# Kernel tuning notes

Measured on AMD Instinct MI355X. Metric: run time of the kernel, lower is better.

The kernel has to match this reference:

```python
import jax, jax.numpy as jnp
import numpy as np

DECAY = 0.99
EPS = 1e-05
DIM = 64
N_EMBED = 512
X_SHAPE = (32, 4096, DIM)


def setup_inputs() -> dict:
    key = jax.random.key(0)
    k1, k2 = jax.random.split(key)
    x = jax.random.normal(k1, X_SHAPE, dtype=jnp.float32)
    # codebook init uniform(-1/n_embed, 1/n_embed), as in torch .uniform_
    embed = jax.random.uniform(k2, (DIM, N_EMBED), dtype=jnp.float32,
                               minval=-1.0 / N_EMBED, maxval=1.0 / N_EMBED)
    cluster_size = jnp.zeros((N_EMBED,), dtype=jnp.float32)
    embed_avg = embed.copy()
    return {"x": x, "embed": embed, "cluster_size": cluster_size, "embed_avg": embed_avg}


def reference(x, embed, cluster_size, embed_avg):
    dim, n_embed = embed.shape
    flatten = x.reshape(-1, dim)  # [N, dim]
    # squared euclidean distance to each code: ||f||^2 - 2 f.E + ||E||^2  -> [N, n_embed]
    dist = (jnp.sum(flatten * flatten, axis=1, keepdims=True)
            - 2.0 * (flatten @ embed)
            + jnp.sum(embed * embed, axis=0, keepdims=True))
    embed_ind_flat = jnp.argmin(dist, axis=1)  # [N]
    embed_ind = embed_ind_flat.reshape(x.shape[:-1])
    quantize = jnp.take(embed.T, embed_ind_flat, axis=0).reshape(x.shape)

    # --- training-mode EMA buffer updates (no gradient flows; torch uses .data) ---
    f_sg = jax.lax.stop_gradient(flatten)
    # onehot.sum(0) == histogram of assignments; flatten.T @ onehot == segment_sum
    onehot_sum = jnp.zeros((n_embed,), dtype=x.dtype).at[embed_ind_flat].add(1.0)
    embed_sum = jax.ops.segment_sum(f_sg, embed_ind_flat, num_segments=n_embed).T  # [dim, n_embed]
    new_cluster_size = cluster_size * DECAY + (1.0 - DECAY) * onehot_sum
    new_embed_avg = embed_avg * DECAY + (1.0 - DECAY) * embed_sum
    n = jnp.sum(new_cluster_size)
    cs = (new_cluster_size + EPS) / (n + n_embed * EPS) * n
    new_embed = new_embed_avg / cs[None, :]

    diff = jnp.mean(jnp.square(jax.lax.stop_gradient(quantize) - x))
    quantize_st = x + jax.lax.stop_gradient(quantize - x)  # straight-through
    return quantize_st, diff, embed_ind, new_embed, new_cluster_size, new_embed_avg
```

## Files before the change

### kernel.cpp

```cpp
#include <hip/hip_runtime.h>

#define NVEC  131072
#define DIM   64
#define K     512
#define DECAYF 0.99f
#define OMDF   0.01f
#define EPSF   1e-5f
#define VPB   128
#define NBLK_ASSIGN (NVEC / VPB)

#define Q_OFF    0
#define DIFF_OFF 8388608
#define IND_OFF  8388609
#define NE_OFF   8519681
#define NCS_OFF  8552449
#define NEA_OFF  8552961

#define ET_OFF    0
#define C_OFF     32768
#define DPART_OFF 33280
#define INDI_OFF  35328
#define PCNT_OFF  166400
#define PESUM_OFF 168448
#define NSH_OFF   299520

__global__ __launch_bounds__(256) void vq_prep(const float* __restrict__ embed,
                                               float* __restrict__ ws) {
    #pragma clang fp contract(off)
    int j = blockIdx.x * 256 + threadIdx.x;
    float c = 0.0f;
    for (int d = 0; d < DIM; ++d) {
        float v = embed[d * K + j];
        ws[ET_OFF + j * DIM + d] = v;
        float t = v * v;
        c = c + t;
    }
    ws[C_OFF + j] = c;
}

__global__ __launch_bounds__(256)
__attribute__((amdgpu_waves_per_eu(3)))
void vq_assign(
    const float* __restrict__ x,
    const float* __restrict__ ET,
    const float* __restrict__ C,
    int*   __restrict__ indI,
    float* __restrict__ dpart,
    float* __restrict__ out)
{
    #pragma clang fp contract(off)
    __shared__ float sda[4][64], sdb[4][64];
    __shared__ int   sia[4][64], sib[4][64];
    __shared__ int   sba[64], sbb[64];
    __shared__ float wdl[4];

    int lane = threadIdx.x & 63;
    int wq   = __builtin_amdgcn_readfirstlane(threadIdx.x >> 6);
    int va   = blockIdx.x * VPB + lane;
    int vb   = va + 64;
    const float* fxa = x + (size_t)va * DIM;
    const float* fxb = x + (size_t)vb * DIM;

    float fa[DIM], fb[DIM];
    #pragma unroll
    for (int k = 0; k < DIM / 4; ++k) {
        float4 t = ((const float4*)fxa)[k];
        fa[4*k+0] = t.x; fa[4*k+1] = t.y; fa[4*k+2] = t.z; fa[4*k+3] = t.w;
    }
    #pragma unroll
    for (int k = 0; k < DIM / 4; ++k) {
        float4 t = ((const float4*)fxb)[k];
        fb[4*k+0] = t.x; fb[4*k+1] = t.y; fb[4*k+2] = t.z; fb[4*k+3] = t.w;
    }

    #define PIN16(a, b) asm volatile("" \
        : "+v"(a[(b)+0]),  "+v"(a[(b)+1]),  "+v"(a[(b)+2]),  "+v"(a[(b)+3]), \
          "+v"(a[(b)+4]),  "+v"(a[(b)+5]),  "+v"(a[(b)+6]),  "+v"(a[(b)+7]), \
          "+v"(a[(b)+8]),  "+v"(a[(b)+9]),  "+v"(a[(b)+10]), "+v"(a[(b)+11]), \
          "+v"(a[(b)+12]), "+v"(a[(b)+13]), "+v"(a[(b)+14]), "+v"(a[(b)+15]))
    PIN16(fa, 0); PIN16(fa, 16); PIN16(fa, 32); PIN16(fa, 48);
    PIN16(fb, 0); PIN16(fb, 16); PIN16(fb, 32); PIN16(fb, 48);
    #undef PIN16

    float ra[8], rb[8];
    #pragma unroll
    for (int k = 0; k < 8; ++k) { ra[k] = fa[k] * fa[k]; rb[k] = fb[k] * fb[k]; }
    #pragma unroll
    for (int b = 1; b < 8; ++b) {
        #pragma unroll
        for (int k = 0; k < 8; ++k) {
            float t0 = fa[8*b + k] * fa[8*b + k];
            ra[k] = ra[k] + t0;
            float t1 = fb[8*b + k] * fb[8*b + k];
            rb[k] = rb[k] + t1;
        }
    }
    float Aa = ((ra[0] + ra[1]) + (ra[2] + ra[3])) + ((ra[4] + ra[5]) + (ra[6] + ra[7]));
    float Ab = ((rb[0] + rb[1]) + (rb[2] + rb[3])) + ((rb[4] + rb[5]) + (rb[6] + rb[7]));

    const float* eseg = ET + (size_t)wq * 128 * DIM;
    const float* Cseg = C + wq * 128;
    float bda = 3.0e38f, bdb = 3.0e38f;
    int   bia = wq * 128, bib = wq * 128;
    #pragma unroll 1
    for (int jj = 0; jj < 128; ++jj) {
        const float* e = eseg + jj * DIM;
        float ma = 0.0f, mb = 0.0f;
        #pragma unroll
        for (int d = 0; d < DIM; ++d) {
            float ev = e[d];
            ma = __builtin_fmaf(fa[d], ev, ma);
            mb = __builtin_fmaf(fb[d], ev, mb);
        }
        int j = wq * 128 + jj;
        float Cv = Cseg[jj];
        float t1a = 2.0f * ma;
        float t2a = Aa - t1a;
        float da  = t2a + Cv;
        float t1b = 2.0f * mb;
        float t2b = Ab - t1b;
        float db  = t2b + Cv;
        if (da < bda) { bda = da; bia = j; }
        if (db < bdb) { bdb = db; bib = j; }
    }

    sda[wq][lane] = bda; sia[wq][lane] = bia;
    sdb[wq][lane] = bdb; sib[wq][lane] = bib;
    __syncthreads();

    if (wq == 0) {
        float bd = sda[0][lane]; int bi = sia[0][lane];
        #pragma unroll
        for (int q = 1; q < 4; ++q) {
            float d2 = sda[q][lane]; int i2 = sia[q][lane];
            if (d2 < bd || (d2 == bd && i2 < bi)) { bd = d2; bi = i2; }
        }
        sba[lane] = bi;
        out[IND_OFF + va] = (float)bi;
        indI[va] = bi;

        bd = sdb[0][lane]; bi = sib[0][lane];
        #pragma unroll
        for (int q = 1; q < 4; ++q) {
            float d2 = sdb[q][lane]; int i2 = sib[q][lane];
            if (d2 < bd || (d2 == bd && i2 < bi)) { bd = d2; bi = i2; }
        }
        sbb[lane] = bi;
        out[IND_OFF + vb] = (float)bi;
        indI[vb] = bi;
    }
    __syncthreads();

    float dl = 0.0f;
    if (wq == 0) {
        int bsel = sba[lane];
        const float4* qr = (const float4*)(ET + (size_t)bsel * DIM);
        float4* orow = (float4*)(out + Q_OFF + (size_t)va * DIM);
        #pragma unroll
        for (int k = 0; k < 16; ++k) {
            float4 tq = qr[k];
            float r0 = tq.x - fa[4*k+0];
            float r1 = tq.y - fa[4*k+1];
            float r2 = tq.z - fa[4*k+2];
            float r3 = tq.w - fa[4*k+3];
            dl = __builtin_fmaf(r0, r0, dl); dl = __builtin_fmaf(r1, r1, dl);
            dl = __builtin_fmaf(r2, r2, dl); dl = __builtin_fmaf(r3, r3, dl);
            orow[k] = tq;
        }
    } else if (wq == 1) {
        int bsel = sbb[lane];
        const float4* qr = (const float4*)(ET + (size_t)bsel * DIM);
        float4* orow = (float4*)(out + Q_OFF + (size_t)vb * DIM);
        #pragma unroll
        for (int k = 0; k < 16; ++k) {
            float4 tq = qr[k];
            float r0 = tq.x - fb[4*k+0];
            float r1 = tq.y - fb[4*k+1];
            float r2 = tq.z - fb[4*k+2];
            float r3 = tq.w - fb[4*k+3];
            dl = __builtin_fmaf(r0, r0, dl); dl = __builtin_fmaf(r1, r1, dl);
            dl = __builtin_fmaf(r2, r2, dl); dl = __builtin_fmaf(r3, r3, dl);
            orow[k] = tq;
        }
    }

    #pragma unroll
    for (int off = 32; off > 0; off >>= 1) dl += __shfl_down(dl, off);
    if (lane == 0) wdl[wq] = dl;
    __syncthreads();
    if (threadIdx.x == 0)
        dpart[blockIdx.x] = ((wdl[0] + wdl[1]) + (wdl[2] + wdl[3]));
}

__global__ __launch_bounds__(512) void vq_stats(
    const float* __restrict__ x,
    const int* __restrict__ indI,
    float* __restrict__ pcnt,
    float* __restrict__ pesum)
{
    __shared__ float p[4][8][DIM];
    __shared__ float c[4][8];
    int jg   = blockIdx.x >> 2;
    int q    = blockIdx.x & 3;
    int lane = threadIdx.x & 63;
    int w    = __builtin_amdgcn_readfirstlane(threadIdx.x >> 6);
    int j0   = jg * 4;

    int seg  = q * 8 + w;
    int base = seg * (NVEC / 32);

    float acc[4] = {0.0f, 0.0f, 0.0f, 0.0f};
    int   cnt[4] = {0, 0, 0, 0};
    for (int i = 0; i < NVEC / 32; i += 256) {
        int4 idv = ((const int4*)(indI + base + i))[lane];
        #pragma unroll
        for (int jj = 0; jj < 4; ++jj) {
            int j = j0 + jj;
            unsigned long long m0 = __ballot(idv.x == j);
            unsigned long long m1 = __ballot(idv.y == j);
            unsigned long long m2 = __ballot(idv.z == j);
            unsigned long long m3 = __ballot(idv.w == j);
            cnt[jj] += (int)(__popcll(m0) + __popcll(m1)
                           + __popcll(m2) + __popcll(m3));
            while (m0) { int b = __builtin_ctzll(m0); m0 &= m0 - 1;
                         acc[jj] += x[(size_t)(base + i + 4*b + 0) * DIM + lane]; }
            while (m1) { int b = __builtin_ctzll(m1); m1 &= m1 - 1;
                         acc[jj] += x[(size_t)(base + i + 4*b + 1) * DIM + lane]; }
            while (m2) { int b = __builtin_ctzll(m2); m2 &= m2 - 1;
                         acc[jj] += x[(size_t)(base + i + 4*b + 2) * DIM + lane]; }
            while (m3) { int b = __builtin_ctzll(m3); m3 &= m3 - 1;
                         acc[jj] += x[(size_t)(base + i + 4*b + 3) * DIM + lane]; }
        }
    }
    #pragma unroll
    for (int jj = 0; jj < 4; ++jj) {
        p[jj][w][lane] = acc[jj];
        if (lane == 0) c[jj][w] = (float)cnt[jj];
    }
    __syncthreads();
    if (w == 0) {
        #pragma unroll
        for (int jj = 0; jj < 4; ++jj) {
            float s = ((p[jj][0][lane] + p[jj][1][lane])
                     + (p[jj][2][lane] + p[jj][3][lane]))
                    + ((p[jj][4][lane] + p[jj][5][lane])
                     + (p[jj][6][lane] + p[jj][7][lane]));
            pesum[((size_t)q * K + (j0 + jj)) * DIM + lane] = s;
            if (lane == 0)
                pcnt[q * K + (j0 + jj)] =
                    ((c[jj][0] + c[jj][1]) + (c[jj][2] + c[jj][3]))
                  + ((c[jj][4] + c[jj][5]) + (c[jj][6] + c[jj][7]));
        }
    }
}

__global__ __launch_bounds__(512) void vq_finalize(
    const float* __restrict__ cluster_size,
    const float* __restrict__ embed_avg,
    const float* __restrict__ ws,
    float* __restrict__ out)
{
    __shared__ float wsum[8];
    __shared__ float dsum_sh[8];
    __shared__ float n_sh;
    int d = blockIdx.x;
    int j = threadIdx.x;

    float cj = ((ws[PCNT_OFF + 0*K + j] + ws[PCNT_OFF + 1*K + j])
              + (ws[PCNT_OFF + 2*K + j] + ws[PCNT_OFF + 3*K + j]));
    float ncs = DECAYF * cluster_size[j] + OMDF * cj;
    if (d == 0) out[NCS_OFF + j] = ncs;

    float dsum = 0.0f;
    if (d == 0) {
        #pragma unroll
        for (int k = 0; k < NBLK_ASSIGN / 512; ++k)
            dsum += ws[DPART_OFF + k * 512 + j];
    }

    float s = ncs;
    #pragma unroll
    for (int off = 32; off > 0; off >>= 1) {
        s    += __shfl_down(s, off);
        dsum += __shfl_down(dsum, off);
    }
    if ((j & 63) == 0) { wsum[j >> 6] = s; dsum_sh[j >> 6] = dsum; }
    __syncthreads();
    if (j == 0) {
        float n = 0.f, dtot = 0.f;
        #pragma unroll
        for (int w = 0; w < 8; ++w) { n += wsum[w]; dtot += dsum_sh[w]; }
        n_sh = n;
        if (d == 0) out[DIFF_OFF] = dtot * (1.0f / 8388608.0f);
    }
    __syncthreads();
    float n   = n_sh;
    float csz = (ncs + EPSF) / (n + (float)K * EPSF) * n;

    float es = ((ws[PESUM_OFF + ((size_t)0*K + j) * DIM + d]
               + ws[PESUM_OFF + ((size_t)1*K + j) * DIM + d])
              + (ws[PESUM_OFF + ((size_t)2*K + j) * DIM + d]
               + ws[PESUM_OFF + ((size_t)3*K + j) * DIM + d]));
    float ea = DECAYF * embed_avg[d * K + j] + OMDF * es;
    out[NEA_OFF + d * K + j] = ea;
    out[NE_OFF  + d * K + j] = ea / csz;
}

extern "C" void kernel_launch(void* const* d_in, const int* in_sizes, int n_in,
                              void* d_out, int out_size, void* d_ws, size_t ws_size,
                              hipStream_t stream) {
    const float* x            = (const float*)d_in[0];
    const float* embed        = (const float*)d_in[1];
    const float* cluster_size = (const float*)d_in[2];
    const float* embed_avg    = (const float*)d_in[3];
    float* out = (float*)d_out;
    float* ws  = (float*)d_ws;
    int*   indI = (int*)(ws + INDI_OFF);

    vq_prep<<<K / 256, 256, 0, stream>>>(embed, ws);
    vq_assign<<<NBLK_ASSIGN, 256, 0, stream>>>(
        x, ws + ET_OFF, ws + C_OFF, indI, ws + DPART_OFF, out);
    vq_stats<<<(K / 4) * 4, 512, 0, stream>>>(
        x, indI, ws + PCNT_OFF, ws + PESUM_OFF);
    vq_finalize<<<DIM, K, 0, stream>>>(cluster_size, embed_avg, ws, out);
}
```

Baseline: 268.8 us.

## Fuse cluster statistics into assign kernel using global atomics

Removes the separate stats kernel that rescanned all assignment indices per code group, and instead has the two idle waves of each assign block atomically add counts and vector sums into zeroed global buffers. The prep kernel now also zeroes those buffers, and finalize reads a single partial instead of four. This drops a kernel launch and the redundant index scans and x re-reads, at the cost of millions of float atomics and a summation order that is no longer deterministic.

```diff
diff --git a/kernel.cpp b/kernel.cpp
--- a/kernel.cpp
+++ b/kernel.cpp
@@ -19,23 +19,28 @@
 #define ET_OFF    0
 #define C_OFF     32768
 #define DPART_OFF 33280
-#define INDI_OFF  35328
 #define PCNT_OFF  166400
-#define PESUM_OFF 168448
-#define NSH_OFF   299520
+#define PESUM_OFF 166912
+#define STATZ_N   (K + K * DIM)
 
 __global__ __launch_bounds__(256) void vq_prep(const float* __restrict__ embed,
                                                float* __restrict__ ws) {
     #pragma clang fp contract(off)
-    int j = blockIdx.x * 256 + threadIdx.x;
-    float c = 0.0f;
-    for (int d = 0; d < DIM; ++d) {
-        float v = embed[d * K + j];
-        ws[ET_OFF + j * DIM + d] = v;
-        float t = v * v;
-        c = c + t;
-    }
-    ws[C_OFF + j] = c;
+    int bid = blockIdx.x;
+    if (bid < 2) {
+        int j = bid * 256 + threadIdx.x;
+        float c = 0.0f;
+        for (int d = 0; d < DIM; ++d) {
+            float v = embed[d * K + j];
+            ws[ET_OFF + j * DIM + d] = v;
+            float t = v * v;
+            c = c + t;
+        }
+        ws[C_OFF + j] = c;
+    } else {
+        int i = (bid - 2) * 256 + threadIdx.x;
+        ws[PCNT_OFF + i] = 0.0f;
+    }
 }
 
 __global__ __launch_bounds__(256)
@@ -44,7 +49,8 @@
     const float* __restrict__ x,
     const float* __restrict__ ET,
     const float* __restrict__ C,
-    int*   __restrict__ indI,
+    float* __restrict__ pcnt,
+    float* __restrict__ pesum,
     float* __restrict__ dpart,
     float* __restrict__ out)
 {
@@ -137,7 +143,6 @@
         }
         sba[lane] = bi;
         out[IND_OFF + va] = (float)bi;
-        indI[va] = bi;
 
         bd = sdb[0][lane]; bi = sib[0][lane];
         #pragma unroll
@@ -147,7 +152,6 @@
         }
         sbb[lane] = bi;
         out[IND_OFF + vb] = (float)bi;
-        indI[vb] = bi;
     }
     __syncthreads();
 
@@ -182,6 +186,24 @@
             dl = __builtin_fmaf(r2, r2, dl); dl = __builtin_fmaf(r3, r3, dl);
             orow[k] = tq;
         }
+    } else if (wq == 2) {
+        atomicAdd(&pcnt[sba[lane]], 1.0f);
+        int base = blockIdx.x * VPB;
+        #pragma unroll 4
+        for (int k = 0; k < 64; ++k) {
+            int bi = sba[k];
+            const float* xr = x + (size_t)(base + k) * DIM;
+            atomicAdd(&pesum[(size_t)bi * DIM + lane], xr[lane]);
+        }
+    } else {
+        atomicAdd(&pcnt[sbb[lane]], 1.0f);
+        int base = blockIdx.x * VPB + 64;
+        #pragma unroll 4
+        for (int k = 0; k < 64; ++k) {
+            int bi = sbb[k];
+            const float* xr = x + (size_t)(base + k) * DIM;
+            atomicAdd(&pesum[(size_t)bi * DIM + lane], xr[lane]);
+        }
     }
 
     #pragma unroll
@@ -190,68 +212,6 @@
     __syncthreads();
     if (threadIdx.x == 0)
         dpart[blockIdx.x] = ((wdl[0] + wdl[1]) + (wdl[2] + wdl[3]));
-}
-
-__global__ __launch_bounds__(512) void vq_stats(
-    const float* __restrict__ x,
-    const int* __restrict__ indI,
-    float* __restrict__ pcnt,
-    float* __restrict__ pesum)
-{
-    __shared__ float p[4][8][DIM];
-    __shared__ float c[4][8];
-    int jg   = blockIdx.x >> 2;
-    int q    = blockIdx.x & 3;
-    int lane = threadIdx.x & 63;
-    int w    = __builtin_amdgcn_readfirstlane(threadIdx.x >> 6);
-    int j0   = jg * 4;
-
-    int seg  = q * 8 + w;
-    int base = seg * (NVEC / 32);
-
-    float acc[4] = {0.0f, 0.0f, 0.0f, 0.0f};
-    int   cnt[4] = {0, 0, 0, 0};
-    for (int i = 0; i < NVEC / 32; i += 256) {
-        int4 idv = ((const int4*)(indI + base + i))[lane];
-        #pragma unroll
-        for (int jj = 0; jj < 4; ++jj) {
-            int j = j0 + jj;
-            unsigned long long m0 = __ballot(idv.x == j);
-            unsigned long long m1 = __ballot(idv.y == j);
-            unsigned long long m2 = __ballot(idv.z == j);
-            unsigned long long m3 = __ballot(idv.w == j);
-            cnt[jj] += (int)(__popcll(m0) + __popcll(m1)
-                           + __popcll(m2) + __popcll(m3));
-            while (m0) { int b = __builtin_ctzll(m0); m0 &= m0 - 1;
-                         acc[jj] += x[(size_t)(base + i + 4*b + 0) * DIM + lane]; }
-            while (m1) { int b = __builtin_ctzll(m1); m1 &= m1 - 1;
-                         acc[jj] += x[(size_t)(base + i + 4*b + 1) * DIM + lane]; }
-            while (m2) { int b = __builtin_ctzll(m2); m2 &= m2 - 1;
-                         acc[jj] += x[(size_t)(base + i + 4*b + 2) * DIM + lane]; }
-            while (m3) { int b = __builtin_ctzll(m3); m3 &= m3 - 1;
-                         acc[jj] += x[(size_t)(base + i + 4*b + 3) * DIM + lane]; }
-        }
-    }
-    #pragma unroll
-    for (int jj = 0; jj < 4; ++jj) {
-        p[jj][w][lane] = acc[jj];
-        if (lane == 0) c[jj][w] = (float)cnt[jj];
-    }
-    __syncthreads();
-    if (w == 0) {
-        #pragma unroll
-        for (int jj = 0; jj < 4; ++jj) {
-            float s = ((p[jj][0][lane] + p[jj][1][lane])
-                     + (p[jj][2][lane] + p[jj][3][lane]))
-                    + ((p[jj][4][lane] + p[jj][5][lane])
-                     + (p[jj][6][lane] + p[jj][7][lane]));
-            pesum[((size_t)q * K + (j0 + jj)) * DIM + lane] = s;
-            if (lane == 0)
-                pcnt[q * K + (j0 + jj)] =
-                    ((c[jj][0] + c[jj][1]) + (c[jj][2] + c[jj][3]))
-                  + ((c[jj][4] + c[jj][5]) + (c[jj][6] + c[jj][7]));
-        }
-    }
 }
 
 __global__ __launch_bounds__(512) void vq_finalize(
@@ -266,8 +226,7 @@
     int d = blockIdx.x;
     int j = threadIdx.x;
 
-    float cj = ((ws[PCNT_OFF + 0*K + j] + ws[PCNT_OFF + 1*K + j])
-              + (ws[PCNT_OFF + 2*K + j] + ws[PCNT_OFF + 3*K + j]));
+    float cj = ws[PCNT_OFF + j];
     float ncs = DECAYF * cluster_size[j] + OMDF * cj;
     if (d == 0) out[NCS_OFF + j] = ncs;
 
@@ -297,10 +256,7 @@
     float n   = n_sh;
     float csz = (ncs + EPSF) / (n + (float)K * EPSF) * n;
 
-    float es = ((ws[PESUM_OFF + ((size_t)0*K + j) * DIM + d]
-               + ws[PESUM_OFF + ((size_t)1*K + j) * DIM + d])
-              + (ws[PESUM_OFF + ((size_t)2*K + j) * DIM + d]
-               + ws[PESUM_OFF + ((size_t)3*K + j) * DIM + d]));
+    float es = ws[PESUM_OFF + (size_t)j * DIM + d];
     float ea = DECAYF * embed_avg[d * K + j] + OMDF * es;
     out[NEA_OFF + d * K + j] = ea;
     out[NE_OFF  + d * K + j] = ea / csz;
@@ -315,12 +271,10 @@
     const float* embed_avg    = (const float*)d_in[3];
     float* out = (float*)d_out;
     float* ws  = (float*)d_ws;
-    int*   indI = (int*)(ws + INDI_OFF);
-
-    vq_prep<<<K / 256, 256, 0, stream>>>(embed, ws);
+
+    vq_prep<<<2 + STATZ_N / 256, 256, 0, stream>>>(embed, ws);
     vq_assign<<<NBLK_ASSIGN, 256, 0, stream>>>(
-        x, ws + ET_OFF, ws + C_OFF, indI, ws + DPART_OFF, out);
-    vq_stats<<<(K / 4) * 4, 512, 0, stream>>>(
-        x, indI, ws + PCNT_OFF, ws + PESUM_OFF);
+        x, ws + ET_OFF, ws + C_OFF, ws + PCNT_OFF, ws + PESUM_OFF,
+        ws + DPART_OFF, out);
     vq_finalize<<<DIM, K, 0, stream>>>(cluster_size, embed_avg, ws, out);
 }
```

Result: slower. 331.5 us (+23.3%).
